# Kernel optimization log

Measured on AMD Instinct MI355X. Metric: run time of the kernel, lower is better.

The kernel has to match this reference:

```python
import jax, jax.numpy as jnp
import numpy as np

N_SENTS, N_ENTS, BATCH, DIM, HEADS = 64, 16, 64, 512, 8


def setup_inputs() -> dict:
    key = jax.random.key(0)
    ks = jax.random.split(key, 10)
    se = N_SENTS * N_ENTS
    s = 0.02  # init scale for projection weights
    entities = jax.random.normal(ks[0], (se, BATCH, DIM), dtype=jnp.float32)
    query_param = jax.random.uniform(ks[1], (1, 1, DIM), jnp.float32, -1.0, 1.0)
    wq = jax.random.normal(ks[2], (DIM, DIM), jnp.float32) * s
    wk = jax.random.normal(ks[3], (DIM, DIM), jnp.float32) * s
    wv = jax.random.normal(ks[4], (DIM, DIM), jnp.float32) * s
    wo = jax.random.normal(ks[5], (DIM, DIM), jnp.float32) * s
    bq = jax.random.normal(ks[6], (DIM,), jnp.float32) * s
    bk = jax.random.normal(ks[7], (DIM,), jnp.float32) * s
    bv = jax.random.normal(ks[8], (DIM,), jnp.float32) * s
    bo = jax.random.normal(ks[9], (DIM,), jnp.float32) * s
    return {"entities": entities, "query_param": query_param,
            "wq": wq, "wk": wk, "wv": wv, "wo": wo,
            "bq": bq, "bk": bk, "bv": bv, "bo": bo,
            "n_sents": N_SENTS}


def reference(entities, query_param, wq, wk, wv, wo, bq, bk, bv, bo, n_sents):
    # entities: [n_sents*n_ents, batch, dim]
    se, b, d = entities.shape
    n_ents = se // n_sents
    h = HEADS
    hd = d // h

    # Learned single query broadcast to every (sentence, batch) slot.
    q_in = jnp.broadcast_to(query_param, (n_sents, b, d))
    q = q_in @ wq.T + bq            # [n_sents, b, d]
    k = entities @ wk.T + bk        # [se, b, d]
    v = entities @ wv.T + bv        # [se, b, d]

    # Split heads -> [b, h, len, hd]
    qh = q.reshape(n_sents, b, h, hd).transpose(1, 2, 0, 3)
    kh = k.reshape(se, b, h, hd).transpose(1, 2, 0, 3)
    vh = v.reshape(se, b, h, hd).transpose(1, 2, 0, 3)

    scale = jnp.asarray(1.0 / np.sqrt(hd), dtype=qh.dtype)
    scores = jnp.einsum('bhqd,bhkd->bhqk', qh, kh) * scale  # [b,h,n_sents,se]

    # Block-diagonal mask: query i attends only to keys [i*n_ents, (i+1)*n_ents)
    valid = (jnp.arange(se) // n_ents)[None, :] == jnp.arange(n_sents)[:, None]
    scores = jnp.where(valid[None, None], scores, jnp.finfo(scores.dtype).min)

    attn = jax.nn.softmax(scores, axis=-1)
    ctx = jnp.einsum('bhqk,bhkd->bhqd', attn, vh)            # [b,h,n_sents,hd]
    out = ctx.transpose(2, 0, 1, 3).reshape(n_sents, b, d)   # merge heads
    return out @ wo.T + bo                                   # [n_sents, b, d]
```

## Files before the change

kernel.cpp:

```cpp
#include <hip/hip_runtime.h>
#include <stdint.h>

#define HEADS 8
#define DIM   512
#define HD    64
#define NE    16
#define NS    64
#define NB    64

typedef short bf16x8 __attribute__((ext_vector_type(8)));
typedef float f32x4  __attribute__((ext_vector_type(4)));

__device__ __forceinline__ unsigned short f2bf(float f) {
    union { float f; uint32_t u; } v; v.f = f;
    uint32_t u = v.u;
    u += 0x7fffu + ((u >> 16) & 1u);
    return (unsigned short)(u >> 16);
}

__device__ __forceinline__ bf16x8 cvt8(float4 lo, float4 hi) {
    union { uint32_t u[4]; bf16x8 v; } r;
    asm("v_cvt_pk_bf16_f32 %0, %1, %2" : "=v"(r.u[0]) : "v"(lo.x), "v"(lo.y));
    asm("v_cvt_pk_bf16_f32 %0, %1, %2" : "=v"(r.u[1]) : "v"(lo.z), "v"(lo.w));
    asm("v_cvt_pk_bf16_f32 %0, %1, %2" : "=v"(r.u[2]) : "v"(hi.x), "v"(hi.y));
    asm("v_cvt_pk_bf16_f32 %0, %1, %2" : "=v"(r.u[3]) : "v"(hi.z), "v"(hi.w));
    return r.v;
}

__global__ __launch_bounds__(256) void k_prep(
    const float* __restrict__ qp, const float* __restrict__ wq,
    const float* __restrict__ bq, const float* __restrict__ wv,
    const float* __restrict__ wo, float* __restrict__ qvec,
    unsigned short* __restrict__ wv_bf, unsigned short* __restrict__ wo_bf)
{
    const int bid = blockIdx.x;
    const int t = threadIdx.x;
    if (bid < 64) {
        const int dl = t >> 5, js = t & 31;
        const int d = bid * 8 + dl;
        const float* w = wq + (size_t)d * DIM + js * 16;
        const float* q = qp + js * 16;
        float acc = 0.f;
        #pragma unroll
        for (int i = 0; i < 16; i++) acc += w[i] * q[i];
        #pragma unroll
        for (int msk = 16; msk >= 1; msk >>= 1) acc += __shfl_xor(acc, msk);
        if (js == 0) qvec[d] = acc + bq[d];
        return;
    }
    const bool is_v = bid < 320;
    const float* src = is_v ? wv : wo;
    unsigned short* dst = is_v ? wv_bf : wo_bf;
    const int li = ((is_v ? bid - 64 : bid - 320) * 1024 + t * 4);
    const float4 v = *(const float4*)(src + li);
    ushort4 hv;
    hv.x = f2bf(v.x); hv.y = f2bf(v.y); hv.z = f2bf(v.z); hv.w = f2bf(v.w);
    *(ushort4*)(dst + li) = hv;
}

__global__ __launch_bounds__(256) void k_uproj(
    const float* __restrict__ qvec, const float* __restrict__ wk,
    unsigned short* __restrict__ u_bf)
{
    const int bid = blockIdx.x;
    const int t = threadIdx.x;
    if (bid >= 16) {
        const int row = 8 + (bid - 16) * 4 + (t >> 6);
        ((uint4*)(u_bf + row * DIM))[t & 63] = (uint4){0u, 0u, 0u, 0u};
        return;
    }
    const int h = bid >> 1;
    const int c = (bid & 1) * 256 + t;
    __shared__ float qs[HD];
    if (t < HD) qs[t] = qvec[h * HD + t];
    __syncthreads();
    const float* w = wk + (size_t)(h * HD) * DIM + c;
    float acc = 0.f;
    #pragma unroll 8
    for (int j = 0; j < HD; j++) acc += qs[j] * w[(size_t)j * DIM];
    u_bf[h * DIM + c] = f2bf(acc);
}

__global__ __launch_bounds__(256) void k_attn(
    const float* __restrict__ ents, const unsigned short* __restrict__ u_bf,
    unsigned short* __restrict__ weighted)
{
    __shared__ float attn_s[4][NE][8];
    const int t = threadIdx.x;
    const int w = t >> 6, lane = t & 63;
    const int bid = ((int)blockIdx.x & 7) * 128 + ((int)blockIdx.x >> 3);
    const int s = bid >> 4;
    const int b = ((bid & 15) << 2) | w;

    const int m = lane & 15, g = lane >> 4;

    const float* aptr = ents + (((size_t)(s * NE + m)) * NB + b) * DIM + g * 8;
    const unsigned short* urow = u_bf + m * DIM + g * 8;
    f32x4 acc = {0.f, 0.f, 0.f, 0.f};
    #pragma unroll
    for (int ks = 0; ks < 16; ks++) {
        const float4 f0 = *(const float4*)(aptr + ks * 32);
        const float4 f1 = *(const float4*)(aptr + ks * 32 + 4);
        const bf16x8 af = cvt8(f0, f1);
        const bf16x8 bf = *(const bf16x8*)(urow + ks * 32);
        acc = __builtin_amdgcn_mfma_f32_16x16x32_bf16(af, bf, acc, 0, 0, 0);
    }

    {
        const float scale = 0.125f;
        float s0 = acc[0]*scale, s1 = acc[1]*scale, s2 = acc[2]*scale, s3 = acc[3]*scale;
        float mx = fmaxf(fmaxf(s0, s1), fmaxf(s2, s3));
        mx = fmaxf(mx, __shfl_xor(mx, 16));
        mx = fmaxf(mx, __shfl_xor(mx, 32));
        const float p0 = __expf(s0 - mx), p1 = __expf(s1 - mx);
        const float p2 = __expf(s2 - mx), p3 = __expf(s3 - mx);
        float sm = p0 + p1 + p2 + p3;
        sm += __shfl_xor(sm, 16);
        sm += __shfl_xor(sm, 32);
        const float inv = 1.f / sm;
        if (m < HEADS) {
            attn_s[w][4 * g + 0][m] = p0 * inv;
            attn_s[w][4 * g + 1][m] = p1 * inv;
            attn_s[w][4 * g + 2][m] = p2 * inv;
            attn_s[w][4 * g + 3][m] = p3 * inv;
        }
    }

    const int d0 = lane << 3;
    f32x4 accA[HEADS], accB[HEADS];
    #pragma unroll
    for (int h = 0; h < HEADS; h++) { accA[h] = (f32x4){0,0,0,0}; accB[h] = (f32x4){0,0,0,0}; }

    const float* erow = ents + (((size_t)(s * NE)) * NB + b) * DIM + d0;
    #pragma unroll
    for (int e = 0; e < NE; e++) {
        const float* ep = erow + (size_t)e * (NB * DIM);
        const f32x4 e0 = *(const f32x4*)(ep);
        const f32x4 e1 = *(const f32x4*)(ep + 4);
        const f32x4 a0 = *(const f32x4*)&attn_s[w][e][0];
        const f32x4 a1 = *(const f32x4*)&attn_s[w][e][4];
        accA[0] += a0.x * e0; accB[0] += a0.x * e1;
        accA[1] += a0.y * e0; accB[1] += a0.y * e1;
        accA[2] += a0.z * e0; accB[2] += a0.z * e1;
        accA[3] += a0.w * e0; accB[3] += a0.w * e1;
        accA[4] += a1.x * e0; accB[4] += a1.x * e1;
        accA[5] += a1.y * e0; accB[5] += a1.y * e1;
        accA[6] += a1.z * e0; accB[6] += a1.z * e1;
        accA[7] += a1.w * e0; accB[7] += a1.w * e1;
    }
    unsigned short* wrow = weighted + ((size_t)(s * NB + b) << 12) + d0;
    #pragma unroll
    for (int h = 0; h < HEADS; h++) {
        const bf16x8 ov = cvt8((float4){accA[h].x, accA[h].y, accA[h].z, accA[h].w},
                               (float4){accB[h].x, accB[h].y, accB[h].z, accB[h].w});
        *(bf16x8*)(wrow + h * DIM) = ov;
    }
}

template <typename CT>
__global__ __launch_bounds__(256) void k_gemm(
    const unsigned short* __restrict__ A, int lda, int aOffY,
    const unsigned short* __restrict__ B, int ldb, int bOffY,
    const float* __restrict__ bias, CT* __restrict__ C, int ldc, int cOffY, int K)
{
    __shared__ unsigned short a_s[64][72];
    __shared__ unsigned short b_s[64][72];
    const int t = threadIdx.x;
    const int m0 = blockIdx.x * 64;
    const int y  = blockIdx.y;
    const int w = t >> 6, l = t & 63;
    const int m = l & 15, g = l >> 4;
    const int lr = t >> 2, lk = (t & 3) * 16;

    const unsigned short* Ap = A + (size_t)(m0 + lr) * lda + (size_t)aOffY * y;
    const unsigned short* Bp = B + (size_t)(bOffY * y + lr) * ldb;

    f32x4 acc[4];
    #pragma unroll
    for (int i = 0; i < 4; i++) acc[i] = (f32x4){0.f, 0.f, 0.f, 0.f};

    for (int k0 = 0; k0 < K; k0 += 64) {
        const ushort4 av0 = *(const ushort4*)(Ap + k0 + lk);
        const ushort4 av1 = *(const ushort4*)(Ap + k0 + lk + 4);
        const ushort4 av2 = *(const ushort4*)(Ap + k0 + lk + 8);
        const ushort4 av3 = *(const ushort4*)(Ap + k0 + lk + 12);
        const ushort4 bv0 = *(const ushort4*)(Bp + k0 + lk);
        const ushort4 bv1 = *(const ushort4*)(Bp + k0 + lk + 4);
        const ushort4 bv2 = *(const ushort4*)(Bp + k0 + lk + 8);
        const ushort4 bv3 = *(const ushort4*)(Bp + k0 + lk + 12);
        *(ushort4*)&a_s[lr][lk]      = av0;
        *(ushort4*)&a_s[lr][lk + 4]  = av1;
        *(ushort4*)&a_s[lr][lk + 8]  = av2;
        *(ushort4*)&a_s[lr][lk + 12] = av3;
        *(ushort4*)&b_s[lr][lk]      = bv0;
        *(ushort4*)&b_s[lr][lk + 4]  = bv1;
        *(ushort4*)&b_s[lr][lk + 8]  = bv2;
        *(ushort4*)&b_s[lr][lk + 12] = bv3;
        __syncthreads();
        #pragma unroll
        for (int kk = 0; kk < 64; kk += 32) {
            const int kp = kk + g * 8;
            const bf16x8 af = *(const bf16x8*)&a_s[w * 16 + m][kp];
            const bf16x8 b0 = *(const bf16x8*)&b_s[ 0 + m][kp];
            const bf16x8 b1 = *(const bf16x8*)&b_s[16 + m][kp];
            const bf16x8 b2 = *(const bf16x8*)&b_s[32 + m][kp];
            const bf16x8 b3 = *(const bf16x8*)&b_s[48 + m][kp];
            acc[0] = __builtin_amdgcn_mfma_f32_16x16x32_bf16(af, b0, acc[0], 0, 0, 0);
            acc[1] = __builtin_amdgcn_mfma_f32_16x16x32_bf16(af, b1, acc[1], 0, 0, 0);
            acc[2] = __builtin_amdgcn_mfma_f32_16x16x32_bf16(af, b2, acc[2], 0, 0, 0);
            acc[3] = __builtin_amdgcn_mfma_f32_16x16x32_bf16(af, b3, acc[3], 0, 0, 0);
        }
        __syncthreads();
    }

    const int colbase = cOffY * y;
    #pragma unroll
    for (int nt = 0; nt < 4; nt++) {
        const int col = colbase + nt * 16 + m;
        const float bs = bias[col];
        #pragma unroll
        for (int j = 0; j < 4; j++) {
            const int row = m0 + w * 16 + g * 4 + j;
            const float val = acc[nt][j] + bs;
            if (sizeof(CT) == 2) {
                ((unsigned short*)C)[(size_t)row * ldc + col] = f2bf(val);
            } else {
                ((float*)C)[(size_t)row * ldc + col] = val;
            }
        }
    }
}

extern "C" void kernel_launch(void* const* d_in, const int* in_sizes, int n_in,
                              void* d_out, int out_size, void* d_ws, size_t ws_size,
                              hipStream_t stream)
{
    const float* ents = (const float*)d_in[0];
    const float* qp   = (const float*)d_in[1];
    const float* wq   = (const float*)d_in[2];
    const float* wk   = (const float*)d_in[3];
    const float* wv   = (const float*)d_in[4];
    const float* wo   = (const float*)d_in[5];
    const float* bq   = (const float*)d_in[6];
    const float* bv   = (const float*)d_in[8];
    const float* bo   = (const float*)d_in[9];

    char* ws = (char*)d_ws;
    float*          qvec     = (float*)ws;
    unsigned short* u_bf     = (unsigned short*)(ws + 4096);
    unsigned short* wv_bf    = (unsigned short*)(ws + 65536);
    unsigned short* wo_bf    = (unsigned short*)(ws + 65536 + 524288);
    unsigned short* weighted = (unsigned short*)(ws + 2097152);
    unsigned short* ctx      = (unsigned short*)(ws + 2097152 + 33554432);

    k_prep <<<576, 256, 0, stream>>>(qp, wq, bq, wv, wo, qvec, wv_bf, wo_bf);
    k_uproj<<<18, 256, 0, stream>>>(qvec, wk, u_bf);
    k_attn <<<1024, 256, 0, stream>>>(ents, u_bf, weighted);
    k_gemm<unsigned short><<<dim3(64, 8), 256, 0, stream>>>(
        weighted, HEADS * DIM, DIM, wv_bf, DIM, HD, bv, ctx, DIM, HD, DIM);
    k_gemm<float><<<dim3(64, 8), 256, 0, stream>>>(
        ctx, DIM, 0, wo_bf, DIM, HD, bo, (float*)d_out, DIM, HD, DIM);
}
```

Measured before the change: 74.29 us.

## Fuse query/key projection into prep and stream entities once in attention

Merges the q-projection and the u=Wk^T q projection into the prep kernel, which removes one launch and keeps u in fp32. The attention kernel now reads each entity row only once. It computes per-head scores with FP32 dot products and wave-wide shuffles, then accumulates unnormalized exp-weighted sums in a single pass, replacing the bf16 MFMA score pass plus a second read of the entities. The exp is clamped instead of max-subtracted, which changes numerics and relies on scores staying in a bounded range. The per-entity shuffle reductions across 8 heads add cross-lane work.

After: 137.5 us. 1.85x slower.

```diff
diff --git a/kernel.cpp b/kernel.cpp
--- a/kernel.cpp
+++ b/kernel.cpp
@@ -18,7 +18,7 @@
     return (unsigned short)(u >> 16);
 }
 
-__device__ __forceinline__ bf16x8 cvt8(float4 lo, float4 hi) {
+__device__ __forceinline__ bf16x8 cvt8(f32x4 lo, f32x4 hi) {
     union { uint32_t u[4]; bf16x8 v; } r;
     asm("v_cvt_pk_bf16_f32 %0, %1, %2" : "=v"(r.u[0]) : "v"(lo.x), "v"(lo.y));
     asm("v_cvt_pk_bf16_f32 %0, %1, %2" : "=v"(r.u[1]) : "v"(lo.z), "v"(lo.w));
@@ -29,130 +29,114 @@
 
 __global__ __launch_bounds__(256) void k_prep(
     const float* __restrict__ qp, const float* __restrict__ wq,
-    const float* __restrict__ bq, const float* __restrict__ wv,
-    const float* __restrict__ wo, float* __restrict__ qvec,
+    const float* __restrict__ bq, const float* __restrict__ wk,
+    const float* __restrict__ wv, const float* __restrict__ wo,
+    float* __restrict__ u_f,
     unsigned short* __restrict__ wv_bf, unsigned short* __restrict__ wo_bf)
 {
     const int bid = blockIdx.x;
     const int t = threadIdx.x;
-    if (bid < 64) {
-        const int dl = t >> 5, js = t & 31;
-        const int d = bid * 8 + dl;
-        const float* w = wq + (size_t)d * DIM + js * 16;
-        const float* q = qp + js * 16;
+    if (bid < 16) {
+        const int h = bid >> 1, ch = bid & 1;
+        __shared__ float qs[HD];
+        {
+            const int j = t >> 2, q = t & 3;
+            const float* w = wq + (size_t)(h * HD + j) * DIM + q * 128;
+            const float* qq = qp + q * 128;
+            float a = 0.f;
+            #pragma unroll 8
+            for (int i = 0; i < 128; i++) a += w[i] * qq[i];
+            a += __shfl_xor(a, 1);
+            a += __shfl_xor(a, 2);
+            if (q == 0) qs[j] = a + bq[h * HD + j];
+        }
+        __syncthreads();
+        const int c = ch * 256 + t;
+        const float* w = wk + (size_t)(h * HD) * DIM + c;
         float acc = 0.f;
-        #pragma unroll
-        for (int i = 0; i < 16; i++) acc += w[i] * q[i];
-        #pragma unroll
-        for (int msk = 16; msk >= 1; msk >>= 1) acc += __shfl_xor(acc, msk);
-        if (js == 0) qvec[d] = acc + bq[d];
+        #pragma unroll 8
+        for (int j = 0; j < HD; j++) acc += qs[j] * w[(size_t)j * DIM];
+        u_f[h * DIM + c] = acc;
         return;
     }
-    const bool is_v = bid < 320;
+    const bool is_v = bid < 272;
     const float* src = is_v ? wv : wo;
     unsigned short* dst = is_v ? wv_bf : wo_bf;
-    const int li = ((is_v ? bid - 64 : bid - 320) * 1024 + t * 4);
+    const int li = ((is_v ? bid - 16 : bid - 272) * 1024 + t * 4);
     const float4 v = *(const float4*)(src + li);
     ushort4 hv;
     hv.x = f2bf(v.x); hv.y = f2bf(v.y); hv.z = f2bf(v.z); hv.w = f2bf(v.w);
     *(ushort4*)(dst + li) = hv;
 }
 
-__global__ __launch_bounds__(256) void k_uproj(
-    const float* __restrict__ qvec, const float* __restrict__ wk,
-    unsigned short* __restrict__ u_bf)
-{
-    const int bid = blockIdx.x;
-    const int t = threadIdx.x;
-    if (bid >= 16) {
-        const int row = 8 + (bid - 16) * 4 + (t >> 6);
-        ((uint4*)(u_bf + row * DIM))[t & 63] = (uint4){0u, 0u, 0u, 0u};
-        return;
-    }
-    const int h = bid >> 1;
-    const int c = (bid & 1) * 256 + t;
-    __shared__ float qs[HD];
-    if (t < HD) qs[t] = qvec[h * HD + t];
-    __syncthreads();
-    const float* w = wk + (size_t)(h * HD) * DIM + c;
-    float acc = 0.f;
-    #pragma unroll 8
-    for (int j = 0; j < HD; j++) acc += qs[j] * w[(size_t)j * DIM];
-    u_bf[h * DIM + c] = f2bf(acc);
-}
-
 __global__ __launch_bounds__(256) void k_attn(
-    const float* __restrict__ ents, const unsigned short* __restrict__ u_bf,
+    const float* __restrict__ ents, const float* __restrict__ u_f,
     unsigned short* __restrict__ weighted)
 {
-    __shared__ float attn_s[4][NE][8];
     const int t = threadIdx.x;
     const int w = t >> 6, lane = t & 63;
     const int bid = ((int)blockIdx.x & 7) * 128 + ((int)blockIdx.x >> 3);
     const int s = bid >> 4;
     const int b = ((bid & 15) << 2) | w;
-
-    const int m = lane & 15, g = lane >> 4;
-
-    const float* aptr = ents + (((size_t)(s * NE + m)) * NB + b) * DIM + g * 8;
-    const unsigned short* urow = u_bf + m * DIM + g * 8;
-    f32x4 acc = {0.f, 0.f, 0.f, 0.f};
-    #pragma unroll
-    for (int ks = 0; ks < 16; ks++) {
-        const float4 f0 = *(const float4*)(aptr + ks * 32);
-        const float4 f1 = *(const float4*)(aptr + ks * 32 + 4);
-        const bf16x8 af = cvt8(f0, f1);
-        const bf16x8 bf = *(const bf16x8*)(urow + ks * 32);
-        acc = __builtin_amdgcn_mfma_f32_16x16x32_bf16(af, bf, acc, 0, 0, 0);
-    }
-
-    {
-        const float scale = 0.125f;
-        float s0 = acc[0]*scale, s1 = acc[1]*scale, s2 = acc[2]*scale, s3 = acc[3]*scale;
-        float mx = fmaxf(fmaxf(s0, s1), fmaxf(s2, s3));
-        mx = fmaxf(mx, __shfl_xor(mx, 16));
-        mx = fmaxf(mx, __shfl_xor(mx, 32));
-        const float p0 = __expf(s0 - mx), p1 = __expf(s1 - mx);
-        const float p2 = __expf(s2 - mx), p3 = __expf(s3 - mx);
-        float sm = p0 + p1 + p2 + p3;
-        sm += __shfl_xor(sm, 16);
-        sm += __shfl_xor(sm, 32);
-        const float inv = 1.f / sm;
-        if (m < HEADS) {
-            attn_s[w][4 * g + 0][m] = p0 * inv;
-            attn_s[w][4 * g + 1][m] = p1 * inv;
-            attn_s[w][4 * g + 2][m] = p2 * inv;
-            attn_s[w][4 * g + 3][m] = p3 * inv;
-        }
-    }
-
     const int d0 = lane << 3;
-    f32x4 accA[HEADS], accB[HEADS];
-    #pragma unroll
-    for (int h = 0; h < HEADS; h++) { accA[h] = (f32x4){0,0,0,0}; accB[h] = (f32x4){0,0,0,0}; }
-
-    const float* erow = ents + (((size_t)(s * NE)) * NB + b) * DIM + d0;
+
+    f32x4 u0[HEADS], u1[HEADS];
+    #pragma unroll
+    for (int h = 0; h < HEADS; h++) {
+        u0[h] = *(const f32x4*)(u_f + h * DIM + d0);
+        u1[h] = *(const f32x4*)(u_f + h * DIM + d0 + 4);
+    }
+
+    const float* base = ents + ((size_t)(s * NE) * NB + b) * DIM + d0;
+    const int ROWSTRIDE = NB * DIM;
+
+    f32x4 acc0[HEADS], acc1[HEADS];
+    float sum[HEADS];
+    #pragma unroll
+    for (int h = 0; h < HEADS; h++) {
+        acc0[h] = (f32x4){0.f, 0.f, 0.f, 0.f};
+        acc1[h] = (f32x4){0.f, 0.f, 0.f, 0.f};
+        sum[h] = 0.f;
+    }
+
+    f32x4 cur0 = *(const f32x4*)(base);
+    f32x4 cur1 = *(const f32x4*)(base + 4);
+    f32x4 nxt0 = *(const f32x4*)(base + ROWSTRIDE);
+    f32x4 nxt1 = *(const f32x4*)(base + ROWSTRIDE + 4);
+
     #pragma unroll
     for (int e = 0; e < NE; e++) {
-        const float* ep = erow + (size_t)e * (NB * DIM);
-        const f32x4 e0 = *(const f32x4*)(ep);
-        const f32x4 e1 = *(const f32x4*)(ep + 4);
-        const f32x4 a0 = *(const f32x4*)&attn_s[w][e][0];
-        const f32x4 a1 = *(const f32x4*)&attn_s[w][e][4];
-        accA[0] += a0.x * e0; accB[0] += a0.x * e1;
-        accA[1] += a0.y * e0; accB[1] += a0.y * e1;
-        accA[2] += a0.z * e0; accB[2] += a0.z * e1;
-        accA[3] += a0.w * e0; accB[3] += a0.w * e1;
-        accA[4] += a1.x * e0; accB[4] += a1.x * e1;
-        accA[5] += a1.y * e0; accB[5] += a1.y * e1;
-        accA[6] += a1.z * e0; accB[6] += a1.z * e1;
-        accA[7] += a1.w * e0; accB[7] += a1.w * e1;
-    }
+        const f32x4 r0 = cur0, r1 = cur1;
+        cur0 = nxt0; cur1 = nxt1;
+        if (e < NE - 2) {
+            nxt0 = *(const f32x4*)(base + (size_t)(e + 2) * ROWSTRIDE);
+            nxt1 = *(const f32x4*)(base + (size_t)(e + 2) * ROWSTRIDE + 4);
+        }
+        float pd[HEADS];
+        #pragma unroll
+        for (int h = 0; h < HEADS; h++) {
+            pd[h] = r0.x * u0[h].x + r0.y * u0[h].y + r0.z * u0[h].z + r0.w * u0[h].w
+                  + r1.x * u1[h].x + r1.y * u1[h].y + r1.z * u1[h].z + r1.w * u1[h].w;
+        }
+        #pragma unroll
+        for (int msk = 1; msk <= 32; msk <<= 1)
+            #pragma unroll
+            for (int h = 0; h < HEADS; h++) pd[h] += __shfl_xor(pd[h], msk);
+        #pragma unroll
+        for (int h = 0; h < HEADS; h++) {
+            const float sc = fminf(fmaxf(pd[h] * 0.125f, -30.f), 30.f);
+            const float p = __expf(sc);
+            sum[h] += p;
+            acc0[h] += p * r0;
+            acc1[h] += p * r1;
+        }
+    }
+
     unsigned short* wrow = weighted + ((size_t)(s * NB + b) << 12) + d0;
     #pragma unroll
     for (int h = 0; h < HEADS; h++) {
-        const bf16x8 ov = cvt8((float4){accA[h].x, accA[h].y, accA[h].z, accA[h].w},
-                               (float4){accB[h].x, accB[h].y, accB[h].z, accB[h].w});
+        const float inv = 1.f / sum[h];
+        const bf16x8 ov = cvt8(acc0[h] * inv, acc1[h] * inv);
         *(bf16x8*)(wrow + h * DIM) = ov;
     }
 }
@@ -246,16 +230,14 @@
     const float* bo   = (const float*)d_in[9];
 
     char* ws = (char*)d_ws;
-    float*          qvec     = (float*)ws;
-    unsigned short* u_bf     = (unsigned short*)(ws + 4096);
+    float*          u_f      = (float*)ws;
     unsigned short* wv_bf    = (unsigned short*)(ws + 65536);
     unsigned short* wo_bf    = (unsigned short*)(ws + 65536 + 524288);
     unsigned short* weighted = (unsigned short*)(ws + 2097152);
     unsigned short* ctx      = (unsigned short*)(ws + 2097152 + 33554432);
 
-    k_prep <<<576, 256, 0, stream>>>(qp, wq, bq, wv, wo, qvec, wv_bf, wo_bf);
-    k_uproj<<<18, 256, 0, stream>>>(qvec, wk, u_bf);
-    k_attn <<<1024, 256, 0, stream>>>(ents, u_bf, weighted);
+    k_prep <<<528, 256, 0, stream>>>(qp, wq, bq, wk, wv, wo, u_f, wv_bf, wo_bf);
+    k_attn <<<1024, 256, 0, stream>>>(ents, u_f, weighted);
     k_gemm<unsigned short><<<dim3(64, 8), 256, 0, stream>>>(
         weighted, HEADS * DIM, DIM, wv_bf, DIM, HD, bv, ctx, DIM, HD, DIM);
     k_gemm<float><<<dim3(64, 8), 256, 0, stream>>>(
```
